# Optimization experiments

Measured on AMD Instinct MI355X. Metric: run time of the kernel, lower is better.

The kernel has to match this reference:

```python
import jax, jax.numpy as jnp
import numpy as np
from jax.scipy.special import logsumexp

B, N, T, D = 32, 400, 315, 512   # batch, fMRI parcels, text/task rows, feature dim
H = 256
EPS = 1e-5                       # InstanceNorm2d default eps
N_ITERS = 100                    # sinkhorn_rpm n_iters


def setup_inputs() -> dict:
    key = jax.random.key(0)
    ks = jax.random.split(key, 6)
    features = jax.random.normal(ks[0], (B, N, D), jnp.float32)
    text = jax.random.normal(ks[1], (T, D), jnp.float32)
    # Affinity bilinear weight, init near identity as in graph-matching Affinity modules
    A = jnp.eye(D, dtype=jnp.float32) + 0.01 * jax.random.normal(ks[2], (D, D), jnp.float32)
    gamma = jnp.ones((), jnp.float32)   # InstanceNorm2d(1, affine=True) weight
    beta = jnp.zeros((), jnp.float32)   # InstanceNorm2d(1, affine=True) bias
    Wh = jax.random.normal(ks[3], (2 * D, H), jnp.float32) / np.float32(np.sqrt(2 * D))
    bh = jnp.zeros((H,), jnp.float32)
    Wo = jax.random.normal(ks[4], (H, 1), jnp.float32) / np.float32(np.sqrt(H))
    bo = jnp.zeros((1,), jnp.float32)
    return {"features": features, "text": text, "A": A, "gamma": gamma,
            "beta": beta, "Wh": Wh, "bh": bh, "Wo": Wo, "bo": bo}


def _forward(features, text, A, gamma, beta, Wh, bh, Wo, bo):
    # Affinity: s[b,n,t] = features[b,n,:] @ A @ text[t,:]   -> [B, N, T]
    s = jnp.einsum('bnd,de,te->bnt', features, A, text)
    # InstanceNorm2d(1, affine): normalize each [N,T] map per batch element (single channel)
    m = jnp.mean(s, axis=(1, 2), keepdims=True)
    v = jnp.var(s, axis=(1, 2), keepdims=True)
    s = gamma * (s - m) * jax.lax.rsqrt(v + EPS) + beta
    # sinkhorn_rpm: log-domain alternating row/col normalization, no slack
    def body(log_a, _):
        log_a = log_a - logsumexp(log_a, axis=2, keepdims=True)  # row normalization
        log_a = log_a - logsumexp(log_a, axis=1, keepdims=True)  # col normalization
        return log_a, None
    log_s, _ = jax.lax.scan(body, s, None, length=N_ITERS)
    s1 = jnp.exp(log_s)                                   # [B, N, T]
    # features_t @ s1, then transpose -> [B, T, D]
    features1 = jnp.einsum('bnd,bnt->btd', features, s1)
    text1 = jnp.broadcast_to(text[None], (features.shape[0], T, D))
    combine = jnp.concatenate([features1, text1], axis=2)  # [B, T, 2D]
    h = jax.nn.relu(combine @ Wh + bh)                     # [B, T, H]
    pred = (h @ Wo + bo)[..., 0]                           # [B, T] == [B, num_tasks]
    return pred


def reference(features, text, A, gamma, beta, Wh, bh, Wo, bo):
    return _forward(features, text, A, gamma, beta, Wh, bh, Wo, bo)
```

## Files before the change

kernel.cpp:

```cpp
#include <hip/hip_runtime.h>
#include <hip/hip_fp16.h>

#define BDIM 32
#define NDIM 400
#define TDIM 315
#define TPAD 320
#define DDIM 512
#define HDIM 256
#define NITER 100

#define OFS_TAB   0u
#define OFS_TB    327680u
#define OFS_STATS 655360u
#define OFS_WHB   655616u
#define OFS_S     1048576u
#define OFS_S1B   9240576u
#define OFS_F1    17432576u
#define OFS_FB    27754496u
#define OFS_THL   OFS_S1B
#define OFS_AHL   (OFS_S1B + 655360u)
#define OFS_WHL   (OFS_S1B + 1703936u)
#define OFS_QPART (OFS_F1 + 4096u)

typedef __attribute__((ext_vector_type(8))) short bf16x8;
typedef __attribute__((ext_vector_type(4))) float f32x4;
typedef unsigned long long ull;

__device__ __forceinline__ unsigned rne_hi(float x) {
  unsigned u = __float_as_uint(x);
  u += 0x7fffu + ((u >> 16) & 1u);
  return u & 0xffff0000u;
}
__device__ __forceinline__ unsigned pack2(float lo, float hi) {
  return (rne_hi(lo) >> 16) | rne_hi(hi);
}
__device__ __forceinline__ unsigned short bf1(float x) { return (unsigned short)(rne_hi(x) >> 16); }
__device__ __forceinline__ float bfres(float x) {
  return x - __uint_as_float(rne_hi(x));
}

template <int CTRL, int RMASK>
__device__ __forceinline__ float dppadd(float x) {
  int y = __builtin_amdgcn_update_dpp(0, __float_as_int(x), CTRL, RMASK, 0xf, true);
  return x + __int_as_float(y);
}
template <int CTRL, int RMASK>
__device__ __forceinline__ float dppmax(float x) {
  int y = __builtin_amdgcn_update_dpp(0, __float_as_int(x), CTRL, RMASK, 0xf, true);
  return fmaxf(x, __int_as_float(y));
}

__global__ void k_pack(const float* __restrict__ F, const float* __restrict__ Wh,
                       const float* __restrict__ text, const float* __restrict__ A,
                       unsigned short* __restrict__ Fb, unsigned short* __restrict__ Whb,
                       unsigned short* __restrict__ tHL, unsigned short* __restrict__ aHL,
                       unsigned short* __restrict__ wHL,
                       float* __restrict__ out, int out_n, float* __restrict__ stats,
                       uint4* __restrict__ qzero) {
  const int NF4 = (BDIM * NDIM * DDIM) / 4;
  const int NW4 = (DDIM * HDIM) / 4;
  const int NT4 = (TPAD * DDIM) / 4;
  const int NTS4 = (TDIM * DDIM) / 4;
  const int NA4 = (DDIM * DDIM) / 4;
  const int NWB4 = (DDIM * HDIM) / 4;
  const int NQ4 = (2 * BDIM * 8 * 320 * 2) / 4;
  int tid0 = blockIdx.x * blockDim.x + threadIdx.x;
  int stride = gridDim.x * blockDim.x;
  for (int i = tid0; i < NF4; i += stride) {
    float4 v = ((const float4*)F)[i];
    ((uint2*)Fb)[i] = make_uint2(pack2(v.x, v.y), pack2(v.z, v.w));
  }
  for (int i = tid0; i < NW4; i += stride) {
    float4 v = ((const float4*)Wh)[i];
    ((uint2*)Whb)[i] = make_uint2(pack2(v.x, v.y), pack2(v.z, v.w));
  }
  for (int i = tid0; i < NT4; i += stride) {
    float4 v = make_float4(0.f, 0.f, 0.f, 0.f);
    if (i < NTS4) v = ((const float4*)text)[i];
    ((uint2*)tHL)[i] = make_uint2(pack2(v.x, v.y), pack2(v.z, v.w));
    ((uint2*)(tHL + TPAD * DDIM))[i] =
        make_uint2(pack2(bfres(v.x), bfres(v.y)), pack2(bfres(v.z), bfres(v.w)));
  }
  for (int i = tid0; i < NA4; i += stride) {
    float4 v = ((const float4*)A)[i];
    ((uint2*)aHL)[i] = make_uint2(pack2(v.x, v.y), pack2(v.z, v.w));
    ((uint2*)(aHL + DDIM * DDIM))[i] =
        make_uint2(pack2(bfres(v.x), bfres(v.y)), pack2(bfres(v.z), bfres(v.w)));
  }
  const float* Wb = Wh + DDIM * HDIM;
  for (int i = tid0; i < NWB4; i += stride) {
    float4 v = ((const float4*)Wb)[i];
    ((uint2*)wHL)[i] = make_uint2(pack2(v.x, v.y), pack2(v.z, v.w));
    ((uint2*)(wHL + DDIM * HDIM))[i] =
        make_uint2(pack2(bfres(v.x), bfres(v.y)), pack2(bfres(v.z), bfres(v.w)));
  }
  for (int i = tid0; i < out_n; i += stride) out[i] = 0.0f;
  for (int i = tid0; i < NQ4; i += stride) qzero[i] = make_uint4(0u, 0u, 0u, 0u);
  if (tid0 < BDIM * 2) stats[tid0] = 0.0f;
}

#define LDH 40

__global__ __launch_bounds__(256) void k_pre(const unsigned short* __restrict__ tHL,
                                             const unsigned short* __restrict__ aHL,
                                             const unsigned short* __restrict__ wHL,
                                             const float* __restrict__ bh,
                                             unsigned short* __restrict__ tAb,
                                             float* __restrict__ TB) {
  __shared__ unsigned short Ahs[64 * LDH], Als[64 * LDH];
  __shared__ unsigned short Bhs[64 * LDH], Bls[64 * LDH];
  const int tid = threadIdx.x, l = tid & 63, wv = tid >> 6;
  const int m = tid >> 2, kq = (tid & 3) * 8;
  const int t0 = blockIdx.y * 64;
  const unsigned short* tH = tHL;
  const unsigned short* tL = tHL + TPAD * DDIM;
  f32x4 acc[4] = {};
  if (blockIdx.z == 0) {
    const int d0 = blockIdx.x * 64;
    const unsigned short* AH = aHL;
    const unsigned short* AL = aHL + DDIM * DDIM;
    for (int k0 = 0; k0 < 512; k0 += 32) {
      *(uint4*)(&Ahs[m * LDH + kq]) = *(const uint4*)(tH + (size_t)(t0 + m) * DDIM + k0 + kq);
      *(uint4*)(&Als[m * LDH + kq]) = *(const uint4*)(tL + (size_t)(t0 + m) * DDIM + k0 + kq);
      *(uint4*)(&Bhs[m * LDH + kq]) = *(const uint4*)(AH + (size_t)(d0 + m) * DDIM + k0 + kq);
      *(uint4*)(&Bls[m * LDH + kq]) = *(const uint4*)(AL + (size_t)(d0 + m) * DDIM + k0 + kq);
      __syncthreads();
      bf16x8 ah = *(const bf16x8*)(&Ahs[(wv * 16 + (l & 15)) * LDH + (l >> 4) * 8]);
      bf16x8 al = *(const bf16x8*)(&Als[(wv * 16 + (l & 15)) * LDH + (l >> 4) * 8]);
#pragma unroll
      for (int c = 0; c < 4; ++c) {
        bf16x8 bh_ = *(const bf16x8*)(&Bhs[(c * 16 + (l & 15)) * LDH + (l >> 4) * 8]);
        bf16x8 bl_ = *(const bf16x8*)(&Bls[(c * 16 + (l & 15)) * LDH + (l >> 4) * 8]);
        acc[c] = __builtin_amdgcn_mfma_f32_16x16x32_bf16(ah, bh_, acc[c], 0, 0, 0);
        acc[c] = __builtin_amdgcn_mfma_f32_16x16x32_bf16(ah, bl_, acc[c], 0, 0, 0);
        acc[c] = __builtin_amdgcn_mfma_f32_16x16x32_bf16(al, bh_, acc[c], 0, 0, 0);
      }
      __syncthreads();
    }
#pragma unroll
    for (int c = 0; c < 4; ++c)
#pragma unroll
      for (int r = 0; r < 4; ++r) {
        int t = t0 + wv * 16 + ((l >> 4) << 2) + r;
        int d = d0 + c * 16 + (l & 15);
        tAb[(size_t)t * DDIM + d] = bf1(acc[c][r]);
      }
  } else {
    if (blockIdx.x >= 4) return;
    const int h0 = blockIdx.x * 64;
    const unsigned short* WH = wHL;
    const unsigned short* WL = wHL + DDIM * HDIM;
    const int col = tid & 31, g = tid >> 5;
    for (int k0 = 0; k0 < 512; k0 += 32) {
      *(uint4*)(&Ahs[m * LDH + kq]) = *(const uint4*)(tH + (size_t)(t0 + m) * DDIM + k0 + kq);
      *(uint4*)(&Als[m * LDH + kq]) = *(const uint4*)(tL + (size_t)(t0 + m) * DDIM + k0 + kq);
      uint4 wh4 = *(const uint4*)(WH + (size_t)(k0 + col) * HDIM + h0 + g * 8);
      uint4 wl4 = *(const uint4*)(WL + (size_t)(k0 + col) * HDIM + h0 + g * 8);
      unsigned short wh8[8], wl8[8];
      *(uint4*)wh8 = wh4;
      *(uint4*)wl8 = wl4;
#pragma unroll
      for (int i = 0; i < 8; ++i) {
        Bhs[(g * 8 + i) * LDH + col] = wh8[i];
        Bls[(g * 8 + i) * LDH + col] = wl8[i];
      }
      __syncthreads();
      bf16x8 ah = *(const bf16x8*)(&Ahs[(wv * 16 + (l & 15)) * LDH + (l >> 4) * 8]);
      bf16x8 al = *(const bf16x8*)(&Als[(wv * 16 + (l & 15)) * LDH + (l >> 4) * 8]);
#pragma unroll
      for (int c = 0; c < 4; ++c) {
        bf16x8 bh_ = *(const bf16x8*)(&Bhs[(c * 16 + (l & 15)) * LDH + (l >> 4) * 8]);
        bf16x8 bl_ = *(const bf16x8*)(&Bls[(c * 16 + (l & 15)) * LDH + (l >> 4) * 8]);
        acc[c] = __builtin_amdgcn_mfma_f32_16x16x32_bf16(ah, bh_, acc[c], 0, 0, 0);
        acc[c] = __builtin_amdgcn_mfma_f32_16x16x32_bf16(ah, bl_, acc[c], 0, 0, 0);
        acc[c] = __builtin_amdgcn_mfma_f32_16x16x32_bf16(al, bh_, acc[c], 0, 0, 0);
      }
      __syncthreads();
    }
#pragma unroll
    for (int c = 0; c < 4; ++c)
#pragma unroll
      for (int r = 0; r < 4; ++r) {
        int t = t0 + wv * 16 + ((l >> 4) << 2) + r;
        int h = h0 + c * 16 + (l & 15);
        TB[(size_t)t * HDIM + h] = acc[c][r] + bh[h];
      }
  }
}

__global__ __launch_bounds__(256) void k_s(const unsigned short* __restrict__ Fb,
                                           const unsigned short* __restrict__ tAb,
                                           __half* __restrict__ s, float* __restrict__ stats) {
  __shared__ unsigned short Abf[64 * LDH];
  __shared__ unsigned short Bbf[64 * LDH];
  __shared__ float red[8];
  const int tid = threadIdx.x, l = tid & 63, wv = tid >> 6;
  const int t0 = blockIdx.x * 64, n0 = blockIdx.y * 64, bz = blockIdx.z;
  const unsigned short* Fbb = Fb + (size_t)bz * NDIM * DDIM;
  __half* sb = s + (size_t)bz * NDIM * TPAD;
  f32x4 acc[4] = {};
  const int m = tid >> 2, kq = (tid & 3) * 8;
  for (int k0 = 0; k0 < 512; k0 += 32) {
    uint4 av = make_uint4(0, 0, 0, 0);
    int n = n0 + m;
    if (n < NDIM) av = *(const uint4*)(Fbb + (size_t)n * DDIM + k0 + kq);
    *(uint4*)(&Abf[m * LDH + kq]) = av;
    uint4 bv = *(const uint4*)(tAb + (size_t)(t0 + m) * DDIM + k0 + kq);
    *(uint4*)(&Bbf[m * LDH + kq]) = bv;
    __syncthreads();
    bf16x8 af = *(const bf16x8*)(&Abf[(wv * 16 + (l & 15)) * LDH + (l >> 4) * 8]);
#pragma unroll
    for (int c = 0; c < 4; ++c) {
      bf16x8 bf_ = *(const bf16x8*)(&Bbf[(c * 16 + (l & 15)) * LDH + (l >> 4) * 8]);
      acc[c] = __builtin_amdgcn_mfma_f32_16x16x32_bf16(af, bf_, acc[c], 0, 0, 0);
    }
    __syncthreads();
  }
  float lsum = 0.f, lsq = 0.f;
#pragma unroll
  for (int c = 0; c < 4; ++c)
#pragma unroll
    for (int r = 0; r < 4; ++r) {
      int n = n0 + wv * 16 + ((l >> 4) << 2) + r;
      int t = t0 + c * 16 + (l & 15);
      if (n < NDIM && t < TDIM) {
        float v = acc[c][r];
        sb[(size_t)n * TPAD + t] = __float2half(v);
        lsum += v;
        lsq = fmaf(v, v, lsq);
      }
    }
#pragma unroll
  for (int mm = 1; mm <= 32; mm <<= 1) {
    lsum += __shfl_xor(lsum, mm, 64);
    lsq += __shfl_xor(lsq, mm, 64);
  }
  if ((tid & 63) == 0) { red[wv * 2] = lsum; red[wv * 2 + 1] = lsq; }
  __syncthreads();
  if (tid == 0) {
    float S = red[0] + red[2] + red[4] + red[6];
    float Q = red[1] + red[3] + red[5] + red[7];
    atomicAdd(&stats[bz * 2], S);
    atomicAdd(&stats[bz * 2 + 1], Q);
  }
}

#define SBLK 8
#define SROWS 50
#define SRPW 10

__global__ __launch_bounds__(320, 1) void k_sinkhorn(const __half* __restrict__ sbuf,
                                                     const float* __restrict__ stats,
                                                     const float* __restrict__ gptr,
                                                     const float* __restrict__ bptr,
                                                     unsigned short* __restrict__ s1b,
                                                     ull* __restrict__ qpart) {
  __shared__ float qpl[5][320];
  __shared__ float qg[5][320];
  const int b = blockIdx.x, c = blockIdx.y;
  const int tid = threadIdx.x, wv = tid >> 6, l = tid & 63;
  const __half* S = sbuf + (size_t)b * NDIM * TPAD;
  unsigned short* S1 = s1b + (size_t)b * NDIM * TPAD;
  const float NT = 400.0f * 315.0f;
  const float mean = stats[2 * b] / NT;
  const float var = stats[2 * b + 1] / NT - mean * mean;
  const float inv = rsqrtf(var + 1e-5f);
  const float alpha = gptr[0] * inv;
  const float L2E = 1.4426950408889634f;
  const float a2 = alpha * L2E;
  const float d2 = (bptr[0] - mean * alpha) * L2E;
  const int r0 = c * SROWS + wv * SRPW;
  const float TOL = 1e-3f;
  const float TN_RATIO = 315.0f / 400.0f;

  float E0[SRPW], E1[SRPW], E2[SRPW], E3[SRPW], E4[SRPW];
#pragma unroll
  for (int j = 0; j < SRPW; ++j) {
    const __half* row = S + (size_t)(r0 + j) * TPAD;
    E0[j] = __builtin_amdgcn_exp2f(fmaf(__half2float(row[l]), a2, d2));
    E1[j] = __builtin_amdgcn_exp2f(fmaf(__half2float(row[64 + l]), a2, d2));
    E2[j] = __builtin_amdgcn_exp2f(fmaf(__half2float(row[128 + l]), a2, d2));
    E3[j] = __builtin_amdgcn_exp2f(fmaf(__half2float(row[192 + l]), a2, d2));
    E4[j] = (l < 59) ? __builtin_amdgcn_exp2f(fmaf(__half2float(row[256 + l]), a2, d2)) : 0.0f;
  }
  float w0 = 1.0f, w1 = 1.0f, w2 = 1.0f, w3 = 1.0f, w4 = (l < 59) ? 1.0f : 0.0f;
  float aj[SRPW];
#pragma unroll
  for (int j = 0; j < SRPW; ++j) aj[j] = 0.0f;

  bool fin = false;
  for (int it = 0; it < NITER; ++it) {
    float p[SRPW];
#pragma unroll
    for (int j = 0; j < SRPW; ++j) {
      float t = E4[j] * w4;
      t = fmaf(E3[j], w3, t);
      t = fmaf(E2[j], w2, t);
      t = fmaf(E1[j], w1, t);
      p[j] = fmaf(E0[j], w0, t);
    }
#pragma unroll
    for (int j = 0; j < SRPW; ++j) p[j] = dppadd<0x111, 0xf>(p[j]);
#pragma unroll
    for (int j = 0; j < SRPW; ++j) p[j] = dppadd<0x112, 0xf>(p[j]);
#pragma unroll
    for (int j = 0; j < SRPW; ++j) p[j] = dppadd<0x114, 0xf>(p[j]);
#pragma unroll
    for (int j = 0; j < SRPW; ++j) p[j] = dppadd<0x118, 0xf>(p[j]);
#pragma unroll
    for (int j = 0; j < SRPW; ++j) p[j] = dppadd<0x142, 0xa>(p[j]);
#pragma unroll
    for (int j = 0; j < SRPW; ++j) p[j] = dppadd<0x143, 0xc>(p[j]);
#pragma unroll
    for (int j = 0; j < SRPW; ++j) {
      float r = __builtin_amdgcn_rcpf(p[j]);
      aj[j] = __int_as_float(__builtin_amdgcn_readlane(__float_as_int(r), 63));
    }
    float q0 = 0.f, q1 = 0.f, q2 = 0.f, q3 = 0.f, q4 = 0.f;
#pragma unroll
    for (int j = 0; j < SRPW; ++j) {
      q0 = fmaf(E0[j], aj[j], q0);
      q1 = fmaf(E1[j], aj[j], q1);
      q2 = fmaf(E2[j], aj[j], q2);
      q3 = fmaf(E3[j], aj[j], q3);
      q4 = fmaf(E4[j], aj[j], q4);
    }
    qpl[wv][l] = q0;
    qpl[wv][64 + l] = q1;
    qpl[wv][128 + l] = q2;
    qpl[wv][192 + l] = q3;
    qpl[wv][256 + l] = q4;
    __syncthreads();
    const int par = it & 1;
    const unsigned tgt = (unsigned)(it + 1);
    ull* bufpar = qpart + ((size_t)par * BDIM + b) * (SBLK * 320);
    if (wv == 0) {
      ull* myp = bufpar + c * 320;
#pragma unroll
      for (int k = 0; k < 5; ++k) {
        int t = k * 64 + l;
        float sm = qpl[0][t] + qpl[1][t] + qpl[2][t] + qpl[3][t] + qpl[4][t];
        __hip_atomic_store(&myp[t], ((ull)tgt << 32) | (ull)__float_as_uint(sm),
                           __ATOMIC_RELAXED, __HIP_MEMORY_SCOPE_AGENT);
      }
    }
    {
      const int ncc = (wv < 3) ? 2 : 1;
      ull got[2][5];
      const int ccs[2] = {wv, wv + 5};
#pragma unroll
      for (int e = 0; e < 2; ++e)
        if (e < ncc && ccs[e] != c) {
#pragma unroll
          for (int k = 0; k < 5; ++k)
            got[e][k] = __hip_atomic_load(&bufpar[ccs[e] * 320 + k * 64 + l],
                                          __ATOMIC_RELAXED, __HIP_MEMORY_SCOPE_AGENT);
        }
      int guard = 0;
      for (;;) {
        bool ok = true;
#pragma unroll
        for (int e = 0; e < 2; ++e)
          if (e < ncc && ccs[e] != c) {
#pragma unroll
            for (int k = 0; k < 5; ++k)
              if ((unsigned)(got[e][k] >> 32) != tgt) {
                got[e][k] = __hip_atomic_load(&bufpar[ccs[e] * 320 + k * 64 + l],
                                              __ATOMIC_RELAXED, __HIP_MEMORY_SCOPE_AGENT);
                ok = false;
              }
          }
        if (ok) break;
        if (++guard > (1 << 20)) break;
      }
      float part[5] = {0.f, 0.f, 0.f, 0.f, 0.f};
#pragma unroll
      for (int e = 0; e < 2; ++e)
        if (e < ncc) {
#pragma unroll
          for (int k = 0; k < 5; ++k) {
            int t = k * 64 + l;
            float v = (ccs[e] == c)
                          ? (qpl[0][t] + qpl[1][t] + qpl[2][t] + qpl[3][t] + qpl[4][t])
                          : __uint_as_float((unsigned)got[e][k]);
            part[k] += v;
          }
        }
#pragma unroll
      for (int k = 0; k < 5; ++k) qg[wv][k * 64 + l] = part[k];
    }
    __syncthreads();
    const float Q0 = qg[0][l] + qg[1][l] + qg[2][l] + qg[3][l] + qg[4][l];
    const float Q1 = qg[0][64 + l] + qg[1][64 + l] + qg[2][64 + l] + qg[3][64 + l] + qg[4][64 + l];
    const float Q2 =
        qg[0][128 + l] + qg[1][128 + l] + qg[2][128 + l] + qg[3][128 + l] + qg[4][128 + l];
    const float Q3 =
        qg[0][192 + l] + qg[1][192 + l] + qg[2][192 + l] + qg[3][192 + l] + qg[4][192 + l];
    const float Q4 =
        qg[0][256 + l] + qg[1][256 + l] + qg[2][256 + l] + qg[3][256 + l] + qg[4][256 + l];
    float r = fabsf(fmaf(Q0 * w0, TN_RATIO, -1.0f));
    r = fmaxf(r, fabsf(fmaf(Q1 * w1, TN_RATIO, -1.0f)));
    r = fmaxf(r, fabsf(fmaf(Q2 * w2, TN_RATIO, -1.0f)));
    r = fmaxf(r, fabsf(fmaf(Q3 * w3, TN_RATIO, -1.0f)));
    if (l < 59) r = fmaxf(r, fabsf(fmaf(Q4 * w4, TN_RATIO, -1.0f)));
    w0 = __builtin_amdgcn_rcpf(Q0);
    w1 = __builtin_amdgcn_rcpf(Q1);
    w2 = __builtin_amdgcn_rcpf(Q2);
    w3 = __builtin_amdgcn_rcpf(Q3);
    if (l < 59) w4 = __builtin_amdgcn_rcpf(Q4);
    if (fin) break;
    r = dppmax<0x111, 0xf>(r);
    r = dppmax<0x112, 0xf>(r);
    r = dppmax<0x114, 0xf>(r);
    r = dppmax<0x118, 0xf>(r);
    r = dppmax<0x142, 0xa>(r);
    r = dppmax<0x143, 0xc>(r);
    const float resid = __int_as_float(__builtin_amdgcn_readlane(__float_as_int(r), 63));
    fin = (resid < TOL) || (it == NITER - 2);
  }

#pragma unroll
  for (int j = 0; j < SRPW; ++j) {
    unsigned short* row = S1 + (size_t)(r0 + j) * TPAD;
    const float a = aj[j];
    row[l] = bf1(a * E0[j] * w0);
    row[64 + l] = bf1(a * E1[j] * w1);
    row[128 + l] = bf1(a * E2[j] * w2);
    row[192 + l] = bf1(a * E3[j] * w3);
    row[256 + l] = (l < 59) ? bf1(a * E4[j] * w4) : (unsigned short)0;
  }
}

__global__ __launch_bounds__(256) void k_f1(const unsigned short* __restrict__ s1b,
                                            const unsigned short* __restrict__ Fb,
                                            unsigned short* __restrict__ f1b) {
  __shared__ unsigned short Abf[64 * LDH];
  __shared__ unsigned short Bbf[64 * LDH];
  const int tid = threadIdx.x, l = tid & 63, wv = tid >> 6;
  const int d0 = blockIdx.x * 64, t0 = blockIdx.y * 64, bz = blockIdx.z;
  const unsigned short* sb = s1b + (size_t)bz * NDIM * TPAD;
  const unsigned short* Fbb = Fb + (size_t)bz * NDIM * DDIM;
  unsigned short* out = f1b + (size_t)bz * TDIM * DDIM;
  f32x4 acc[4] = {};
  const int col = tid & 31, g = tid >> 5;
  for (int k0 = 0; k0 < 416; k0 += 32) {
    int n = k0 + col;
    uint4 av = make_uint4(0, 0, 0, 0), bv = av;
    if (n < NDIM) {
      av = *(const uint4*)(sb + (size_t)n * TPAD + t0 + g * 8);
      bv = *(const uint4*)(Fbb + (size_t)n * DDIM + d0 + g * 8);
    }
    unsigned short ah[8], bh8[8];
    *(uint4*)ah = av;
    *(uint4*)bh8 = bv;
#pragma unroll
    for (int i = 0; i < 8; ++i) {
      Abf[(g * 8 + i) * LDH + col] = ah[i];
      Bbf[(g * 8 + i) * LDH + col] = bh8[i];
    }
    __syncthreads();
    bf16x8 af = *(const bf16x8*)(&Abf[(wv * 16 + (l & 15)) * LDH + (l >> 4) * 8]);
#pragma unroll
    for (int c = 0; c < 4; ++c) {
      bf16x8 bf_ = *(const bf16x8*)(&Bbf[(c * 16 + (l & 15)) * LDH + (l >> 4) * 8]);
      acc[c] = __builtin_amdgcn_mfma_f32_16x16x32_bf16(af, bf_, acc[c], 0, 0, 0);
    }
    __syncthreads();
  }
#pragma unroll
  for (int c = 0; c < 4; ++c)
#pragma unroll
    for (int r = 0; r < 4; ++r) {
      int t = t0 + wv * 16 + ((l >> 4) << 2) + r;
      int d = d0 + c * 16 + (l & 15);
      if (t < TDIM) out[(size_t)t * DDIM + d] = bf1(acc[c][r]);
    }
}

__global__ __launch_bounds__(256) void k_hp(const unsigned short* __restrict__ f1b,
                                            const unsigned short* __restrict__ Whb,
                                            const float* __restrict__ TB,
                                            const float* __restrict__ Wo,
                                            const float* __restrict__ bo,
                                            float* __restrict__ out) {
  __shared__ unsigned short Abf[64 * LDH];
  __shared__ unsigned short Bbf[64 * LDH];
  __shared__ float Wos[64];
  const int tid = threadIdx.x, l = tid & 63, wv = tid >> 6;
  const int j0 = blockIdx.x * 64, r0 = blockIdx.y * 64;
  const int RTOT = BDIM * TDIM;
  if (tid < 64) Wos[tid] = Wo[j0 + tid];
  f32x4 acc[4] = {};
  const int m = tid >> 2, kq = (tid & 3) * 8;
  const int col = tid & 31, g = tid >> 5;
  for (int k0 = 0; k0 < 512; k0 += 32) {
    uint4 av = make_uint4(0, 0, 0, 0);
    int r = r0 + m;
    if (r < RTOT) av = *(const uint4*)(f1b + (size_t)r * DDIM + k0 + kq);
    *(uint4*)(&Abf[m * LDH + kq]) = av;
    uint4 bv = *(const uint4*)(Whb + (size_t)(k0 + col) * HDIM + j0 + g * 8);
    unsigned short bh8[8];
    *(uint4*)bh8 = bv;
#pragma unroll
    for (int i = 0; i < 8; ++i) Bbf[(g * 8 + i) * LDH + col] = bh8[i];
    __syncthreads();
    bf16x8 af = *(const bf16x8*)(&Abf[(wv * 16 + (l & 15)) * LDH + (l >> 4) * 8]);
#pragma unroll
    for (int c = 0; c < 4; ++c) {
      bf16x8 bf_ = *(const bf16x8*)(&Bbf[(c * 16 + (l & 15)) * LDH + (l >> 4) * 8]);
      acc[c] = __builtin_amdgcn_mfma_f32_16x16x32_bf16(af, bf_, acc[c], 0, 0, 0);
    }
    __syncthreads();
  }
  int tmod[4];
#pragma unroll
  for (int r = 0; r < 4; ++r) {
    int rr = r0 + wv * 16 + ((l >> 4) << 2) + r;
    tmod[r] = rr % TDIM;
  }
  float part[4] = {0.f, 0.f, 0.f, 0.f};
#pragma unroll
  for (int c = 0; c < 4; ++c) {
    int jl = c * 16 + (l & 15);
    float woc = Wos[jl];
#pragma unroll
    for (int r = 0; r < 4; ++r) {
      float v = acc[c][r] + TB[(size_t)tmod[r] * HDIM + j0 + jl];
      part[r] = fmaf(fmaxf(v, 0.f), woc, part[r]);
    }
  }
#pragma unroll
  for (int r = 0; r < 4; ++r) part[r] = dppadd<0x111, 0xf>(part[r]);
#pragma unroll
  for (int r = 0; r < 4; ++r) part[r] = dppadd<0x112, 0xf>(part[r]);
#pragma unroll
  for (int r = 0; r < 4; ++r) part[r] = dppadd<0x114, 0xf>(part[r]);
#pragma unroll
  for (int r = 0; r < 4; ++r) part[r] = dppadd<0x118, 0xf>(part[r]);
  if ((l & 15) == 15) {
    float base = (j0 == 0) ? bo[0] : 0.0f;
#pragma unroll
    for (int r = 0; r < 4; ++r) {
      int rr = r0 + wv * 16 + ((l >> 4) << 2) + r;
      if (rr < RTOT) atomicAdd(&out[rr], part[r] + base);
    }
  }
}

extern "C" void kernel_launch(void* const* d_in, const int* in_sizes, int n_in,
                              void* d_out, int out_size, void* d_ws, size_t ws_size,
                              hipStream_t stream) {
  const float* F     = (const float*)d_in[0];
  const float* text  = (const float*)d_in[1];
  const float* A     = (const float*)d_in[2];
  const float* gamma = (const float*)d_in[3];
  const float* beta  = (const float*)d_in[4];
  const float* Wh    = (const float*)d_in[5];
  const float* bh    = (const float*)d_in[6];
  const float* Wo    = (const float*)d_in[7];
  const float* bo    = (const float*)d_in[8];
  float* out = (float*)d_out;
  char* ws = (char*)d_ws;
  unsigned short* tAb = (unsigned short*)(ws + OFS_TAB);
  float* TB    = (float*)(ws + OFS_TB);
  float* stats = (float*)(ws + OFS_STATS);
  unsigned short* Whb = (unsigned short*)(ws + OFS_WHB);
  __half* sbuf = (__half*)(ws + OFS_S);
  unsigned short* s1b = (unsigned short*)(ws + OFS_S1B);
  unsigned short* f1b = (unsigned short*)(ws + OFS_F1);
  unsigned short* Fb  = (unsigned short*)(ws + OFS_FB);
  unsigned short* tHL = (unsigned short*)(ws + OFS_THL);
  unsigned short* aHL = (unsigned short*)(ws + OFS_AHL);
  unsigned short* wHL = (unsigned short*)(ws + OFS_WHL);
  ull* qpart = (ull*)(ws + OFS_QPART);

  k_pack<<<512, 256, 0, stream>>>(F, Wh, text, A, Fb, Whb, tHL, aHL, wHL,
                                  out, out_size, stats, (uint4*)qpart);
  k_pre<<<dim3(8, 5, 2), 256, 0, stream>>>(tHL, aHL, wHL, bh, tAb, TB);
  k_s<<<dim3(5, 7, 32), 256, 0, stream>>>(Fb, tAb, sbuf, stats);
  k_sinkhorn<<<dim3(BDIM, SBLK), 320, 0, stream>>>(sbuf, stats, gamma, beta, s1b, qpart);
  k_f1<<<dim3(8, 5, 32), 256, 0, stream>>>(s1b, Fb, f1b);
  k_hp<<<dim3(4, 158), 256, 0, stream>>>(f1b, Whb, TB, Wo, bo, out);
}
```

Measured before the change: 188.4 us.

## Merge pack and precompute kernels, widen head tile, reorder grid dims

The separate packing kernel and precompute kernel become one launch. Blocks 0-59 convert text, A and Wh to hi/lo bf16 on the fly inside the GEMM tiles, and the remaining blocks pack F and Wh and zero the scratch buffers. The regression head kernel now computes all 256 hidden columns per block, so it writes outputs directly instead of using atomics and no longer needs the output zeroed first. Grid dimensions for k_s and k_f1 are permuted so that the batch index is on x. Together these cut a launch and the intermediate hi/lo buffers, in exchange for more LDS and more registers in the head kernel (16 accumulators).

```diff
diff --git a/kernel.cpp b/kernel.cpp
--- a/kernel.cpp
+++ b/kernel.cpp
@@ -17,9 +17,6 @@
 #define OFS_S1B   9240576u
 #define OFS_F1    17432576u
 #define OFS_FB    27754496u
-#define OFS_THL   OFS_S1B
-#define OFS_AHL   (OFS_S1B + 655360u)
-#define OFS_WHL   (OFS_S1B + 1703936u)
 #define OFS_QPART (OFS_F1 + 4096u)
 
 typedef __attribute__((ext_vector_type(8))) short bf16x8;
@@ -50,80 +47,66 @@
   return fmaxf(x, __int_as_float(y));
 }
 
-__global__ void k_pack(const float* __restrict__ F, const float* __restrict__ Wh,
-                       const float* __restrict__ text, const float* __restrict__ A,
-                       unsigned short* __restrict__ Fb, unsigned short* __restrict__ Whb,
-                       unsigned short* __restrict__ tHL, unsigned short* __restrict__ aHL,
-                       unsigned short* __restrict__ wHL,
-                       float* __restrict__ out, int out_n, float* __restrict__ stats,
-                       uint4* __restrict__ qzero) {
-  const int NF4 = (BDIM * NDIM * DDIM) / 4;
-  const int NW4 = (DDIM * HDIM) / 4;
-  const int NT4 = (TPAD * DDIM) / 4;
-  const int NTS4 = (TDIM * DDIM) / 4;
-  const int NA4 = (DDIM * DDIM) / 4;
-  const int NWB4 = (DDIM * HDIM) / 4;
-  const int NQ4 = (2 * BDIM * 8 * 320 * 2) / 4;
-  int tid0 = blockIdx.x * blockDim.x + threadIdx.x;
-  int stride = gridDim.x * blockDim.x;
-  for (int i = tid0; i < NF4; i += stride) {
-    float4 v = ((const float4*)F)[i];
-    ((uint2*)Fb)[i] = make_uint2(pack2(v.x, v.y), pack2(v.z, v.w));
-  }
-  for (int i = tid0; i < NW4; i += stride) {
-    float4 v = ((const float4*)Wh)[i];
-    ((uint2*)Whb)[i] = make_uint2(pack2(v.x, v.y), pack2(v.z, v.w));
-  }
-  for (int i = tid0; i < NT4; i += stride) {
-    float4 v = make_float4(0.f, 0.f, 0.f, 0.f);
-    if (i < NTS4) v = ((const float4*)text)[i];
-    ((uint2*)tHL)[i] = make_uint2(pack2(v.x, v.y), pack2(v.z, v.w));
-    ((uint2*)(tHL + TPAD * DDIM))[i] =
-        make_uint2(pack2(bfres(v.x), bfres(v.y)), pack2(bfres(v.z), bfres(v.w)));
-  }
-  for (int i = tid0; i < NA4; i += stride) {
-    float4 v = ((const float4*)A)[i];
-    ((uint2*)aHL)[i] = make_uint2(pack2(v.x, v.y), pack2(v.z, v.w));
-    ((uint2*)(aHL + DDIM * DDIM))[i] =
-        make_uint2(pack2(bfres(v.x), bfres(v.y)), pack2(bfres(v.z), bfres(v.w)));
-  }
-  const float* Wb = Wh + DDIM * HDIM;
-  for (int i = tid0; i < NWB4; i += stride) {
-    float4 v = ((const float4*)Wb)[i];
-    ((uint2*)wHL)[i] = make_uint2(pack2(v.x, v.y), pack2(v.z, v.w));
-    ((uint2*)(wHL + DDIM * HDIM))[i] =
-        make_uint2(pack2(bfres(v.x), bfres(v.y)), pack2(bfres(v.z), bfres(v.w)));
-  }
-  for (int i = tid0; i < out_n; i += stride) out[i] = 0.0f;
-  for (int i = tid0; i < NQ4; i += stride) qzero[i] = make_uint4(0u, 0u, 0u, 0u);
-  if (tid0 < BDIM * 2) stats[tid0] = 0.0f;
-}
-
 #define LDH 40
 
-__global__ __launch_bounds__(256) void k_pre(const unsigned short* __restrict__ tHL,
-                                             const unsigned short* __restrict__ aHL,
-                                             const unsigned short* __restrict__ wHL,
-                                             const float* __restrict__ bh,
-                                             unsigned short* __restrict__ tAb,
-                                             float* __restrict__ TB) {
+__global__ __launch_bounds__(256) void k_prep(const float* __restrict__ F,
+                                              const float* __restrict__ Wh,
+                                              const float* __restrict__ text,
+                                              const float* __restrict__ A,
+                                              const float* __restrict__ bh,
+                                              unsigned short* __restrict__ Fb,
+                                              unsigned short* __restrict__ Whb,
+                                              unsigned short* __restrict__ tAb,
+                                              float* __restrict__ TB,
+                                              float* __restrict__ stats,
+                                              uint4* __restrict__ qzero) {
   __shared__ unsigned short Ahs[64 * LDH], Als[64 * LDH];
   __shared__ unsigned short Bhs[64 * LDH], Bls[64 * LDH];
-  const int tid = threadIdx.x, l = tid & 63, wv = tid >> 6;
+  const int bid = blockIdx.x, tid = threadIdx.x;
+  if (bid >= 60) {
+    const int NF4 = (BDIM * NDIM * DDIM) / 4;
+    const int NW4 = (DDIM * HDIM) / 4;
+    const int NQ4 = (2 * BDIM * 8 * 320 * 2) / 4;
+    const int gid = (bid - 60) * 256 + tid;
+    const int stride = 452 * 256;
+    for (int i = gid; i < NF4; i += stride) {
+      float4 v = ((const float4*)F)[i];
+      ((uint2*)Fb)[i] = make_uint2(pack2(v.x, v.y), pack2(v.z, v.w));
+    }
+    for (int i = gid; i < NW4; i += stride) {
+      float4 v = ((const float4*)Wh)[i];
+      ((uint2*)Whb)[i] = make_uint2(pack2(v.x, v.y), pack2(v.z, v.w));
+    }
+    for (int i = gid; i < NQ4; i += stride) qzero[i] = make_uint4(0u, 0u, 0u, 0u);
+    if (gid < BDIM * 2) stats[gid] = 0.0f;
+    return;
+  }
+  const int l = tid & 63, wv = tid >> 6;
   const int m = tid >> 2, kq = (tid & 3) * 8;
-  const int t0 = blockIdx.y * 64;
-  const unsigned short* tH = tHL;
-  const unsigned short* tL = tHL + TPAD * DDIM;
   f32x4 acc[4] = {};
-  if (blockIdx.z == 0) {
-    const int d0 = blockIdx.x * 64;
-    const unsigned short* AH = aHL;
-    const unsigned short* AL = aHL + DDIM * DDIM;
+  if (bid < 40) {
+    const int d0 = (bid & 7) * 64, t0 = (bid >> 3) * 64;
     for (int k0 = 0; k0 < 512; k0 += 32) {
-      *(uint4*)(&Ahs[m * LDH + kq]) = *(const uint4*)(tH + (size_t)(t0 + m) * DDIM + k0 + kq);
-      *(uint4*)(&Als[m * LDH + kq]) = *(const uint4*)(tL + (size_t)(t0 + m) * DDIM + k0 + kq);
-      *(uint4*)(&Bhs[m * LDH + kq]) = *(const uint4*)(AH + (size_t)(d0 + m) * DDIM + k0 + kq);
-      *(uint4*)(&Bls[m * LDH + kq]) = *(const uint4*)(AL + (size_t)(d0 + m) * DDIM + k0 + kq);
+      {
+        int t = t0 + m;
+        float4 v0 = make_float4(0.f, 0.f, 0.f, 0.f), v1 = v0;
+        if (t < TDIM) {
+          v0 = *(const float4*)(text + (size_t)t * DDIM + k0 + kq);
+          v1 = *(const float4*)(text + (size_t)t * DDIM + k0 + kq + 4);
+        }
+        *(uint4*)(&Ahs[m * LDH + kq]) =
+            make_uint4(pack2(v0.x, v0.y), pack2(v0.z, v0.w), pack2(v1.x, v1.y), pack2(v1.z, v1.w));
+        *(uint4*)(&Als[m * LDH + kq]) =
+            make_uint4(pack2(bfres(v0.x), bfres(v0.y)), pack2(bfres(v0.z), bfres(v0.w)),
+                       pack2(bfres(v1.x), bfres(v1.y)), pack2(bfres(v1.z), bfres(v1.w)));
+        float4 w0 = *(const float4*)(A + (size_t)(d0 + m) * DDIM + k0 + kq);
+        float4 w1 = *(const float4*)(A + (size_t)(d0 + m) * DDIM + k0 + kq + 4);
+        *(uint4*)(&Bhs[m * LDH + kq]) =
+            make_uint4(pack2(w0.x, w0.y), pack2(w0.z, w0.w), pack2(w1.x, w1.y), pack2(w1.z, w1.w));
+        *(uint4*)(&Bls[m * LDH + kq]) =
+            make_uint4(pack2(bfres(w0.x), bfres(w0.y)), pack2(bfres(w0.z), bfres(w0.w)),
+                       pack2(bfres(w1.x), bfres(w1.y)), pack2(bfres(w1.z), bfres(w1.w)));
+      }
       __syncthreads();
       bf16x8 ah = *(const bf16x8*)(&Ahs[(wv * 16 + (l & 15)) * LDH + (l >> 4) * 8]);
       bf16x8 al = *(const bf16x8*)(&Als[(wv * 16 + (l & 15)) * LDH + (l >> 4) * 8]);
@@ -146,23 +129,31 @@
         tAb[(size_t)t * DDIM + d] = bf1(acc[c][r]);
       }
   } else {
-    if (blockIdx.x >= 4) return;
-    const int h0 = blockIdx.x * 64;
-    const unsigned short* WH = wHL;
-    const unsigned short* WL = wHL + DDIM * HDIM;
+    const int idx = bid - 40;
+    const int h0 = (idx & 3) * 64, t0 = (idx >> 2) * 64;
+    const float* Wb = Wh + DDIM * HDIM;
     const int col = tid & 31, g = tid >> 5;
     for (int k0 = 0; k0 < 512; k0 += 32) {
-      *(uint4*)(&Ahs[m * LDH + kq]) = *(const uint4*)(tH + (size_t)(t0 + m) * DDIM + k0 + kq);
-      *(uint4*)(&Als[m * LDH + kq]) = *(const uint4*)(tL + (size_t)(t0 + m) * DDIM + k0 + kq);
-      uint4 wh4 = *(const uint4*)(WH + (size_t)(k0 + col) * HDIM + h0 + g * 8);
-      uint4 wl4 = *(const uint4*)(WL + (size_t)(k0 + col) * HDIM + h0 + g * 8);
-      unsigned short wh8[8], wl8[8];
-      *(uint4*)wh8 = wh4;
-      *(uint4*)wl8 = wl4;
-#pragma unroll
-      for (int i = 0; i < 8; ++i) {
-        Bhs[(g * 8 + i) * LDH + col] = wh8[i];
-        Bls[(g * 8 + i) * LDH + col] = wl8[i];
+      {
+        int t = t0 + m;
+        float4 v0 = make_float4(0.f, 0.f, 0.f, 0.f), v1 = v0;
+        if (t < TDIM) {
+          v0 = *(const float4*)(text + (size_t)t * DDIM + k0 + kq);
+          v1 = *(const float4*)(text + (size_t)t * DDIM + k0 + kq + 4);
+        }
+        *(uint4*)(&Ahs[m * LDH + kq]) =
+            make_uint4(pack2(v0.x, v0.y), pack2(v0.z, v0.w), pack2(v1.x, v1.y), pack2(v1.z, v1.w));
+        *(uint4*)(&Als[m * LDH + kq]) =
+            make_uint4(pack2(bfres(v0.x), bfres(v0.y)), pack2(bfres(v0.z), bfres(v0.w)),
+                       pack2(bfres(v1.x), bfres(v1.y)), pack2(bfres(v1.z), bfres(v1.w)));
+        float4 w0 = *(const float4*)(Wb + (size_t)(k0 + col) * HDIM + h0 + g * 8);
+        float4 w1 = *(const float4*)(Wb + (size_t)(k0 + col) * HDIM + h0 + g * 8 + 4);
+        float wr[8] = {w0.x, w0.y, w0.z, w0.w, w1.x, w1.y, w1.z, w1.w};
+#pragma unroll
+        for (int i = 0; i < 8; ++i) {
+          Bhs[(g * 8 + i) * LDH + col] = bf1(wr[i]);
+          Bls[(g * 8 + i) * LDH + col] = bf1(bfres(wr[i]));
+        }
       }
       __syncthreads();
       bf16x8 ah = *(const bf16x8*)(&Ahs[(wv * 16 + (l & 15)) * LDH + (l >> 4) * 8]);
@@ -195,7 +186,7 @@
   __shared__ unsigned short Bbf[64 * LDH];
   __shared__ float red[8];
   const int tid = threadIdx.x, l = tid & 63, wv = tid >> 6;
-  const int t0 = blockIdx.x * 64, n0 = blockIdx.y * 64, bz = blockIdx.z;
+  const int bz = blockIdx.x, t0 = blockIdx.y * 64, n0 = blockIdx.z * 64;
   const unsigned short* Fbb = Fb + (size_t)bz * NDIM * DDIM;
   __half* sb = s + (size_t)bz * NDIM * TPAD;
   f32x4 acc[4] = {};
@@ -437,7 +428,7 @@
   __shared__ unsigned short Abf[64 * LDH];
   __shared__ unsigned short Bbf[64 * LDH];
   const int tid = threadIdx.x, l = tid & 63, wv = tid >> 6;
-  const int d0 = blockIdx.x * 64, t0 = blockIdx.y * 64, bz = blockIdx.z;
+  const int bz = blockIdx.x, d0 = blockIdx.y * 64, t0 = blockIdx.z * 64;
   const unsigned short* sb = s1b + (size_t)bz * NDIM * TPAD;
   const unsigned short* Fbb = Fb + (size_t)bz * NDIM * DDIM;
   unsigned short* out = f1b + (size_t)bz * TDIM * DDIM;
@@ -484,13 +475,13 @@
                                             const float* __restrict__ bo,
                                             float* __restrict__ out) {
   __shared__ unsigned short Abf[64 * LDH];
-  __shared__ unsigned short Bbf[64 * LDH];
-  __shared__ float Wos[64];
+  __shared__ unsigned short Bbf[256 * LDH];
+  __shared__ float Wos[256];
   const int tid = threadIdx.x, l = tid & 63, wv = tid >> 6;
-  const int j0 = blockIdx.x * 64, r0 = blockIdx.y * 64;
+  const int r0 = blockIdx.x * 64;
   const int RTOT = BDIM * TDIM;
-  if (tid < 64) Wos[tid] = Wo[j0 + tid];
-  f32x4 acc[4] = {};
+  Wos[tid] = Wo[tid];
+  f32x4 acc[16] = {};
   const int m = tid >> 2, kq = (tid & 3) * 8;
   const int col = tid & 31, g = tid >> 5;
   for (int k0 = 0; k0 < 512; k0 += 32) {
@@ -498,15 +489,18 @@
     int r = r0 + m;
     if (r < RTOT) av = *(const uint4*)(f1b + (size_t)r * DDIM + k0 + kq);
     *(uint4*)(&Abf[m * LDH + kq]) = av;
-    uint4 bv = *(const uint4*)(Whb + (size_t)(k0 + col) * HDIM + j0 + g * 8);
-    unsigned short bh8[8];
-    *(uint4*)bh8 = bv;
-#pragma unroll
-    for (int i = 0; i < 8; ++i) Bbf[(g * 8 + i) * LDH + col] = bh8[i];
+#pragma unroll
+    for (int p = 0; p < 4; ++p) {
+      uint4 bv = *(const uint4*)(Whb + (size_t)(k0 + col) * HDIM + p * 64 + g * 8);
+      unsigned short bh8[8];
+      *(uint4*)bh8 = bv;
+#pragma unroll
+      for (int i = 0; i < 8; ++i) Bbf[(p * 64 + g * 8 + i) * LDH + col] = bh8[i];
+    }
     __syncthreads();
     bf16x8 af = *(const bf16x8*)(&Abf[(wv * 16 + (l & 15)) * LDH + (l >> 4) * 8]);
 #pragma unroll
-    for (int c = 0; c < 4; ++c) {
+    for (int c = 0; c < 16; ++c) {
       bf16x8 bf_ = *(const bf16x8*)(&Bbf[(c * 16 + (l & 15)) * LDH + (l >> 4) * 8]);
       acc[c] = __builtin_amdgcn_mfma_f32_16x16x32_bf16(af, bf_, acc[c], 0, 0, 0);
     }
@@ -520,12 +514,12 @@
   }
   float part[4] = {0.f, 0.f, 0.f, 0.f};
 #pragma unroll
-  for (int c = 0; c < 4; ++c) {
+  for (int c = 0; c < 16; ++c) {
     int jl = c * 16 + (l & 15);
     float woc = Wos[jl];
 #pragma unroll
     for (int r = 0; r < 4; ++r) {
-      float v = acc[c][r] + TB[(size_t)tmod[r] * HDIM + j0 + jl];
+      float v = acc[c][r] + TB[(size_t)tmod[r] * HDIM + jl];
       part[r] = fmaf(fmaxf(v, 0.f), woc, part[r]);
     }
   }
@@ -538,11 +532,11 @@
 #pragma unroll
   for (int r = 0; r < 4; ++r) part[r] = dppadd<0x118, 0xf>(part[r]);
   if ((l & 15) == 15) {
-    float base = (j0 == 0) ? bo[0] : 0.0f;
+    const float base = bo[0];
 #pragma unroll
     for (int r = 0; r < 4; ++r) {
       int rr = r0 + wv * 16 + ((l >> 4) << 2) + r;
-      if (rr < RTOT) atomicAdd(&out[rr], part[r] + base);
+      if (rr < RTOT) out[rr] = part[r] + base;
     }
   }
 }
@@ -569,16 +563,11 @@
   unsigned short* s1b = (unsigned short*)(ws + OFS_S1B);
   unsigned short* f1b = (unsigned short*)(ws + OFS_F1);
   unsigned short* Fb  = (unsigned short*)(ws + OFS_FB);
-  unsigned short* tHL = (unsigned short*)(ws + OFS_THL);
-  unsigned short* aHL = (unsigned short*)(ws + OFS_AHL);
-  unsigned short* wHL = (unsigned short*)(ws + OFS_WHL);
   ull* qpart = (ull*)(ws + OFS_QPART);
 
-  k_pack<<<512, 256, 0, stream>>>(F, Wh, text, A, Fb, Whb, tHL, aHL, wHL,
-                                  out, out_size, stats, (uint4*)qpart);
-  k_pre<<<dim3(8, 5, 2), 256, 0, stream>>>(tHL, aHL, wHL, bh, tAb, TB);
-  k_s<<<dim3(5, 7, 32), 256, 0, stream>>>(Fb, tAb, sbuf, stats);
+  k_prep<<<512, 256, 0, stream>>>(F, Wh, text, A, bh, Fb, Whb, tAb, TB, stats, (uint4*)qpart);
+  k_s<<<dim3(32, 5, 7), 256, 0, stream>>>(Fb, tAb, sbuf, stats);
   k_sinkhorn<<<dim3(BDIM, SBLK), 320, 0, stream>>>(sbuf, stats, gamma, beta, s1b, qpart);
-  k_f1<<<dim3(8, 5, 32), 256, 0, stream>>>(s1b, Fb, f1b);
-  k_hp<<<dim3(4, 158), 256, 0, stream>>>(f1b, Whb, TB, Wo, bo, out);
-}
+  k_f1<<<dim3(32, 8, 5), 256, 0, stream>>>(s1b, Fb, f1b);
+  k_hp<<<dim3(158), 256, 0, stream>>>(f1b, Whb, TB, Wo, bo, out);
+}
```

Result: slower. 196.3 us (+4.2%).
